# Kernel tuning notes

Hardware: AMD Instinct MI355X
Metric: run time of the kernel (lower is better)

The kernel has to match this reference:

```python
import jax, jax.numpy as jnp
import numpy as np

MODEL_DIM = 1024
HEAD_DIM = 64
BATCH = 4
SEQ = 4096


def setup_inputs() -> dict:
    key = jax.random.key(0)
    ks = jax.random.split(key, 7)
    s = 1.0 / np.sqrt(MODEL_DIM)
    x = jax.random.normal(ks[0], (BATCH, SEQ, MODEL_DIM), dtype=jnp.float32)
    # causal lower-triangular boolean mask, broadcast over batch
    mask = jnp.tril(jnp.ones((SEQ, SEQ), dtype=jnp.bool_))
    Wk = jax.random.uniform(ks[1], (MODEL_DIM, HEAD_DIM), jnp.float32, -s, s)
    bk = jax.random.uniform(ks[2], (HEAD_DIM,), jnp.float32, -s, s)
    Wq = jax.random.uniform(ks[3], (MODEL_DIM, HEAD_DIM), jnp.float32, -s, s)
    bq = jax.random.uniform(ks[4], (HEAD_DIM,), jnp.float32, -s, s)
    Wv = jax.random.uniform(ks[5], (MODEL_DIM, HEAD_DIM), jnp.float32, -s, s)
    bv = jax.random.uniform(ks[6], (HEAD_DIM,), jnp.float32, -s, s)
    return {"x": x, "mask": mask, "Wk": Wk, "bk": bk, "Wq": Wq, "bq": bq, "Wv": Wv, "bv": bv}


def reference(x, mask, Wk, bk, Wq, bq, Wv, bv):
    # K, Q, V: (B, S, Dh)
    K = jnp.einsum('bsd,dh->bsh', x, Wk) + bk
    Q = jnp.einsum('bsd,dh->bsh', x, Wq) + bq
    V = jnp.einsum('bsd,dh->bsh', x, Wv) + bv
    scale = 1.0 / jnp.sqrt(jnp.asarray(HEAD_DIM, dtype=x.dtype))
    G = jnp.einsum('bqh,bkh->bqk', Q, K) * scale  # (B, S, S)
    G = jnp.where(mask[None, :, :], G, -jnp.inf)
    G = jax.nn.softmax(G, axis=-1)
    # dropout is identity at inference (eval mode)
    attn = jnp.einsum('bqk,bkh->bqh', G, V)
    return attn
```

## Files before the change

kernel.cpp:

```cpp
#include <hip/hip_runtime.h>
#include <hip/hip_bf16.h>
#include <stdint.h>

typedef __attribute__((ext_vector_type(8))) short bf16x8;
typedef __attribute__((ext_vector_type(4))) short bf16x4;
typedef __attribute__((ext_vector_type(4))) float f32x4;
typedef __attribute__((ext_vector_type(4))) unsigned short us4;

#define MFMA32(a, b, c) __builtin_amdgcn_mfma_f32_16x16x32_bf16(a, b, c, 0, 0, 0)

#if defined(__has_builtin) && __has_builtin(__builtin_amdgcn_mfma_f32_16x16x16bf16_1k)
__device__ __forceinline__ f32x4 MFMA16(bf16x4 a, bf16x4 b, f32x4 c) {
    return __builtin_amdgcn_mfma_f32_16x16x16bf16_1k(a, b, c, 0, 0, 0);
}
#elif defined(__has_builtin) && __has_builtin(__builtin_amdgcn_mfma_f32_16x16x16_bf16)
__device__ __forceinline__ f32x4 MFMA16(bf16x4 a, bf16x4 b, f32x4 c) {
    return __builtin_amdgcn_mfma_f32_16x16x16_bf16(a, b, c, 0, 0, 0);
}
#else
__device__ __forceinline__ f32x4 MFMA16(bf16x4 a, bf16x4 b, f32x4 c) {
    f32x4 d;
    asm volatile("v_mfma_f32_16x16x16_bf16 %0, %1, %2, %3\n\ts_nop 7\n\ts_nop 2"
                 : "=v"(d) : "v"(a), "v"(b), "v"(c));
    return d;
}
#endif

__device__ __forceinline__ short f2bf(float f) {
    union { float f; uint32_t u; } v; v.f = f;
    uint32_t u = v.u;
    u = (u + 0x7FFFu + ((u >> 16) & 1u)) >> 16;
    return (short)u;
}

__device__ __forceinline__ uint32_t cvt_pk_bf16(float lo, float hi) {
    uint32_t r;
    asm("v_cvt_pk_bf16_f32 %0, %1, %2" : "=v"(r) : "v"(lo), "v"(hi));
    return r;
}

#define QSCALE 0.18033688011112042f

__global__ void wt_prep(const float* __restrict__ Wk, const float* __restrict__ bk,
                        const float* __restrict__ Wq, const float* __restrict__ bq,
                        const float* __restrict__ Wv, const float* __restrict__ bv,
                        short* __restrict__ WT, float* __restrict__ biasC) {
    int i = blockIdx.x * 256 + threadIdx.x;
    if (i < 192 * 1024) {
        int c = i >> 10, k = i & 1023, cc = c & 63;
        const float* W; float sc;
        if (c < 64)       { W = Wq; sc = QSCALE; }
        else if (c < 128) { W = Wk; sc = 1.0f;   }
        else              { W = Wv; sc = 1.0f;   }
        WT[i] = f2bf(W[k * 64 + cc] * sc);
    }
    if (blockIdx.x == 0 && threadIdx.x < 192) {
        int c = threadIdx.x;
        float bb;
        if (c < 64)       bb = bq[c] * QSCALE;
        else if (c < 128) bb = bk[c - 64];
        else              bb = bv[c - 128];
        biasC[c] = bb;
    }
}

__global__ __launch_bounds__(256, 4) void qkv_proj(
        const float* __restrict__ X, const short* __restrict__ WT,
        const float* __restrict__ biasC,
        short* __restrict__ Qb, short* __restrict__ Kb, short* __restrict__ Vt) {
    const int lane = threadIdx.x & 63, w = threadIdx.x >> 6;
    const int l15 = lane & 15, h = lane >> 4;
    const int row0 = blockIdx.x * 16;
    const int k0 = w * 256 + h * 8;

    f32x4 acc[12];
#pragma unroll
    for (int t = 0; t < 12; t++) acc[t] = (f32x4){0.f, 0.f, 0.f, 0.f};

    const float* xb = X + (size_t)(row0 + l15) * 1024 + k0;
    const short* wb = WT + (size_t)l15 * 1024 + k0;

    for (int kc = 0; kc < 256; kc += 32) {
        const float4 a0 = *(const float4*)(xb + kc);
        const float4 a1 = *(const float4*)(xb + kc + 4);
        bf16x8 af;
        af[0] = f2bf(a0.x); af[1] = f2bf(a0.y); af[2] = f2bf(a0.z); af[3] = f2bf(a0.w);
        af[4] = f2bf(a1.x); af[5] = f2bf(a1.y); af[6] = f2bf(a1.z); af[7] = f2bf(a1.w);
#pragma unroll
        for (int ct = 0; ct < 12; ct++) {
            bf16x8 bf = *(const bf16x8*)(wb + (size_t)ct * 16 * 1024 + kc);
            acc[ct] = MFMA32(af, bf, acc[ct]);
        }
    }

    __shared__ float buf[4][12][16][17];
#pragma unroll
    for (int ct = 0; ct < 12; ct++)
#pragma unroll
        for (int r = 0; r < 4; r++)
            buf[w][ct][h * 4 + r][l15] = acc[ct][r];
    __syncthreads();

    const int b = row0 >> 12, srow = row0 & 4095;

#pragma unroll
    for (int i = 0; i < 8; i++) {
        const int e = threadIdx.x + 256 * i;
        const int ct = e >> 8, row = (e >> 4) & 15, col = e & 15;
        float val = buf[0][ct][row][col] + buf[1][ct][row][col]
                  + buf[2][ct][row][col] + buf[3][ct][row][col]
                  + biasC[ct * 16 + col];
        if (ct < 4) Qb[(size_t)(row0 + row) * 64 + ct * 16 + col] = f2bf(val);
        else        Kb[(size_t)(row0 + row) * 64 + (ct - 4) * 16 + col] = f2bf(val);
    }
    {
        const int ctv = (threadIdx.x >> 4) & 3;
        const int col = threadIdx.x & 15;
        const int rg = threadIdx.x >> 6;
        const int hd = ctv * 16 + col;
        const float bias = biasC[128 + hd];
        us4 pk;
#pragma unroll
        for (int r = 0; r < 4; r++) {
            const int row = rg * 4 + r;
            float val = buf[0][8 + ctv][row][col] + buf[1][8 + ctv][row][col]
                      + buf[2][8 + ctv][row][col] + buf[3][8 + ctv][row][col] + bias;
            pk[r] = (unsigned short)f2bf(val);
        }
        *(us4*)(Vt + ((size_t)(b * 64 + hd)) * 4096 + srow + rg * 4) = pk;
    }
}

__device__ __forceinline__ void softmax_update(const f32x4 s[4], float& m, float& l,
                                               f32x4 o[4], bf16x4 pb[4]) {
    float mx = s[0][0];
#pragma unroll
    for (int c = 0; c < 4; c++)
#pragma unroll
        for (int r = 0; r < 4; r++) mx = fmaxf(mx, s[c][r]);
    mx = fmaxf(mx, __shfl_xor(mx, 16));
    mx = fmaxf(mx, __shfl_xor(mx, 32));
    const float mn = fmaxf(m, mx);
    const float fac = exp2f(m - mn);
    m = mn;
    float p[4][4];
    float sum = 0.f;
#pragma unroll
    for (int c = 0; c < 4; c++)
#pragma unroll
        for (int r = 0; r < 4; r++) { p[c][r] = exp2f(s[c][r] - mn); sum += p[c][r]; }
    sum += __shfl_xor(sum, 16);
    sum += __shfl_xor(sum, 32);
    l = l * fac + sum;
#pragma unroll
    for (int c = 0; c < 4; c++) o[c] *= fac;
#pragma unroll
    for (int c = 0; c < 4; c++) {
        union { bf16x4 v; uint32_t u[2]; } pk;
        pk.u[0] = cvt_pk_bf16(p[c][0], p[c][1]);
        pk.u[1] = cvt_pk_bf16(p[c][2], p[c][3]);
        pb[c] = pk.v;
    }
}

__global__ __launch_bounds__(256, 3) void attn(
        const short* __restrict__ Qb, const short* __restrict__ Kb,
        const short* __restrict__ Vt, float* __restrict__ out) {
    const int lane = threadIdx.x & 63, wg = threadIdx.x >> 6;
    const int l15 = lane & 15, h = lane >> 4;
    const int g = blockIdx.x;
    const int b = g >> 7;
    const int i = g & 127;
    const int u = (i & 1) ? (127 - (i >> 1)) : (i >> 1);
    const int row32 = u * 32;
    const int lt = u >> 1;
    const size_t bbase = (size_t)b * 4096 * 64;

    const short* qp0 = Qb + bbase + (size_t)(row32 + l15) * 64 + h * 8;
    const short* qp1 = qp0 + 16 * 64;
    const bf16x8 q00 = *(const bf16x8*)qp0,  q01 = *(const bf16x8*)(qp0 + 32);
    const bf16x8 q10 = *(const bf16x8*)qp1,  q11 = *(const bf16x8*)(qp1 + 32);

    f32x4 o0[4], o1[4];
    float m0 = -__builtin_inff(), m1 = -__builtin_inff(), l0 = 0.f, l1 = 0.f;
#pragma unroll
    for (int t = 0; t < 4; t++) { o0[t] = (f32x4){0,0,0,0}; o1[t] = (f32x4){0,0,0,0}; }

    for (int kt = wg; kt <= lt; kt += 4) {
        const short* kb = Kb + bbase + (size_t)kt * 64 * 64;
        f32x4 s0[4], s1[4];
#pragma unroll
        for (int c = 0; c < 4; c++) {
            const short* kp = kb + (size_t)(c * 16 + l15) * 64 + h * 8;
            const bf16x8 kf0 = *(const bf16x8*)kp;
            const bf16x8 kf1 = *(const bf16x8*)(kp + 32);
            f32x4 z = (f32x4){0,0,0,0};
            z = MFMA32(kf0, q00, z);  s0[c] = MFMA32(kf1, q01, z);
            z = (f32x4){0,0,0,0};
            z = MFMA32(kf0, q10, z);  s1[c] = MFMA32(kf1, q11, z);
        }
        if (kt == lt) {
            const int q0g = row32 + l15, q1g = q0g + 16;
#pragma unroll
            for (int c = 0; c < 4; c++) {
#pragma unroll
                for (int r = 0; r < 4; r++) {
                    const int key = kt * 64 + c * 16 + h * 4 + r;
                    if (key > q0g) s0[c][r] = -1e30f;
                    if (key > q1g) s1[c][r] = -1e30f;
                }
            }
        }
        bf16x4 pb0[4], pb1[4];
        softmax_update(s0, m0, l0, o0, pb0);
        softmax_update(s1, m1, l1, o1, pb1);

        const short* vb = Vt + (size_t)b * 64 * 4096 + kt * 64;
#pragma unroll
        for (int ct = 0; ct < 4; ct++) {
            const short* vp = vb + (size_t)(ct * 16 + l15) * 4096 + h * 4;
#pragma unroll
            for (int c = 0; c < 4; c++) {
                const bf16x4 vf = *(const bf16x4*)(vp + c * 16);
                o0[ct] = MFMA16(vf, pb0[c], o0[ct]);
                o1[ct] = MFMA16(vf, pb1[c], o1[ct]);
            }
        }
    }

    __shared__ float c_m[4][32], c_l[4][32];
    __shared__ float c_o[4][64][33];
    if (h == 0) {
        c_m[wg][l15] = m0;  c_m[wg][16 + l15] = m1;
        c_l[wg][l15] = l0;  c_l[wg][16 + l15] = l1;
    }
#pragma unroll
    for (int ct = 0; ct < 4; ct++)
#pragma unroll
        for (int r = 0; r < 4; r++) {
            c_o[wg][ct * 16 + h * 4 + r][l15]      = o0[ct][r];
            c_o[wg][ct * 16 + h * 4 + r][16 + l15] = o1[ct][r];
        }
    __syncthreads();

#pragma unroll
    for (int it = 0; it < 8; it++) {
        const int e = threadIdx.x + 256 * it;
        const int q = e >> 6, d = e & 63;
        const float M = fmaxf(fmaxf(c_m[0][q], c_m[1][q]), fmaxf(c_m[2][q], c_m[3][q]));
        float L = 0.f, V = 0.f;
#pragma unroll
        for (int ww = 0; ww < 4; ww++) {
            const float ee = exp2f(c_m[ww][q] - M);
            L += ee * c_l[ww][q];
            V += ee * c_o[ww][d][q];
        }
        out[bbase + (size_t)(row32 + q) * 64 + d] = V / L;
    }
}

extern "C" void kernel_launch(void* const* d_in, const int* in_sizes, int n_in,
                              void* d_out, int out_size, void* d_ws, size_t ws_size,
                              hipStream_t stream) {
    const float* x  = (const float*)d_in[0];
    const float* Wk = (const float*)d_in[2];
    const float* bk = (const float*)d_in[3];
    const float* Wq = (const float*)d_in[4];
    const float* bq = (const float*)d_in[5];
    const float* Wv = (const float*)d_in[6];
    const float* bv = (const float*)d_in[7];
    float* out = (float*)d_out;

    char* ws = (char*)d_ws;
    short* WT    = (short*)(ws);
    float* biasC = (float*)(ws + 393216);
    short* Qb    = (short*)(ws + (size_t)1 * (1 << 20));
    short* Kb    = (short*)(ws + (size_t)3 * (1 << 20));
    short* Vt    = (short*)(ws + (size_t)5 * (1 << 20));

    wt_prep<<<768, 256, 0, stream>>>(Wk, bk, Wq, bq, Wv, bv, WT, biasC);
    qkv_proj<<<1024, 256, 0, stream>>>(x, WT, biasC, Qb, Kb, Vt);
    attn<<<512, 256, 0, stream>>>(Qb, Kb, Vt, out);
}
```

Measured before the change: 157.7 us.

## Split attention KV range across blocks with separate merge kernel; stage X in LDS

The attention kernel now splits long causal rows into up to four KV chunks of 16 tiles each, launching 1280 blocks whose partial outputs (bf16), maxima and sums are written to workspace and combined by a new attn_merge kernel. This balances work across CUs, since the longest query rows no longer pin a single block. qkv_proj now converts the X tile to bf16 once into shared memory with packed cvt instructions instead of per-wave conversion, and the launch-bounds occupancy hints are dropped. The cost is an extra kernel launch, extra global traffic for partials, and bf16 rounding of partial outputs.

New measurement: 135.0 us. -14.4%, faster.

```diff
diff --git a/kernel.cpp b/kernel.cpp
--- a/kernel.cpp
+++ b/kernel.cpp
@@ -32,7 +32,10 @@
     u = (u + 0x7FFFu + ((u >> 16) & 1u)) >> 16;
     return (short)u;
 }
-
+__device__ __forceinline__ float bf2f(short s) {
+    union { uint32_t u; float f; } v; v.u = ((uint32_t)(unsigned short)s) << 16;
+    return v.f;
+}
 __device__ __forceinline__ uint32_t cvt_pk_bf16(float lo, float hi) {
     uint32_t r;
     asm("v_cvt_pk_bf16_f32 %0, %1, %2" : "=v"(r) : "v"(lo), "v"(hi));
@@ -64,67 +67,85 @@
     }
 }
 
-__global__ __launch_bounds__(256, 4) void qkv_proj(
+__global__ __launch_bounds__(256) void qkv_proj(
         const float* __restrict__ X, const short* __restrict__ WT,
         const float* __restrict__ biasC,
         short* __restrict__ Qb, short* __restrict__ Kb, short* __restrict__ Vt) {
-    const int lane = threadIdx.x & 63, w = threadIdx.x >> 6;
-    const int l15 = lane & 15, h = lane >> 4;
+    union SM {
+        short stage[16][1032];
+        float merge[12][16][4][17];
+    };
+    __shared__ SM sm;
+    const int t = threadIdx.x;
+    const int lane = t & 63, w = t >> 6, l15 = lane & 15, h = lane >> 4;
     const int row0 = blockIdx.x * 16;
-    const int k0 = w * 256 + h * 8;
+
+    {
+        const int srow = t >> 4, sl = t & 15;
+        const float* xr = X + (size_t)(row0 + srow) * 1024 + sl * 8;
+        short* dr = &sm.stage[srow][sl * 8];
+#pragma unroll
+        for (int it = 0; it < 8; it++) {
+            const float4 a0 = *(const float4*)(xr + it * 128);
+            const float4 a1 = *(const float4*)(xr + it * 128 + 4);
+            uint4 pk;
+            pk.x = cvt_pk_bf16(a0.x, a0.y);
+            pk.y = cvt_pk_bf16(a0.z, a0.w);
+            pk.z = cvt_pk_bf16(a1.x, a1.y);
+            pk.w = cvt_pk_bf16(a1.z, a1.w);
+            *(uint4*)(dr + it * 128) = pk;
+        }
+    }
+    __syncthreads();
 
     f32x4 acc[12];
 #pragma unroll
-    for (int t = 0; t < 12; t++) acc[t] = (f32x4){0.f, 0.f, 0.f, 0.f};
-
-    const float* xb = X + (size_t)(row0 + l15) * 1024 + k0;
-    const short* wb = WT + (size_t)l15 * 1024 + k0;
+    for (int ct = 0; ct < 12; ct++) acc[ct] = (f32x4){0.f, 0.f, 0.f, 0.f};
+
+    const short* ar = &sm.stage[l15][w * 256 + h * 8];
+    const short* wb = WT + (size_t)l15 * 1024 + w * 256 + h * 8;
 
     for (int kc = 0; kc < 256; kc += 32) {
-        const float4 a0 = *(const float4*)(xb + kc);
-        const float4 a1 = *(const float4*)(xb + kc + 4);
-        bf16x8 af;
-        af[0] = f2bf(a0.x); af[1] = f2bf(a0.y); af[2] = f2bf(a0.z); af[3] = f2bf(a0.w);
-        af[4] = f2bf(a1.x); af[5] = f2bf(a1.y); af[6] = f2bf(a1.z); af[7] = f2bf(a1.w);
+        const bf16x8 af = *(const bf16x8*)(ar + kc);
 #pragma unroll
         for (int ct = 0; ct < 12; ct++) {
-            bf16x8 bf = *(const bf16x8*)(wb + (size_t)ct * 16 * 1024 + kc);
+            const bf16x8 bf = *(const bf16x8*)(wb + (size_t)ct * 16 * 1024 + kc);
             acc[ct] = MFMA32(af, bf, acc[ct]);
         }
     }
-
-    __shared__ float buf[4][12][16][17];
+    __syncthreads();
+
 #pragma unroll
     for (int ct = 0; ct < 12; ct++)
 #pragma unroll
         for (int r = 0; r < 4; r++)
-            buf[w][ct][h * 4 + r][l15] = acc[ct][r];
+            sm.merge[ct][h * 4 + r][w][l15] = acc[ct][r];
     __syncthreads();
 
     const int b = row0 >> 12, srow = row0 & 4095;
 
 #pragma unroll
     for (int i = 0; i < 8; i++) {
-        const int e = threadIdx.x + 256 * i;
+        const int e = t + 256 * i;
         const int ct = e >> 8, row = (e >> 4) & 15, col = e & 15;
-        float val = buf[0][ct][row][col] + buf[1][ct][row][col]
-                  + buf[2][ct][row][col] + buf[3][ct][row][col]
+        float val = sm.merge[ct][row][0][col] + sm.merge[ct][row][1][col]
+                  + sm.merge[ct][row][2][col] + sm.merge[ct][row][3][col]
                   + biasC[ct * 16 + col];
         if (ct < 4) Qb[(size_t)(row0 + row) * 64 + ct * 16 + col] = f2bf(val);
         else        Kb[(size_t)(row0 + row) * 64 + (ct - 4) * 16 + col] = f2bf(val);
     }
     {
-        const int ctv = (threadIdx.x >> 4) & 3;
-        const int col = threadIdx.x & 15;
-        const int rg = threadIdx.x >> 6;
+        const int ctv = (t >> 4) & 3;
+        const int col = t & 15;
+        const int rg = t >> 6;
         const int hd = ctv * 16 + col;
         const float bias = biasC[128 + hd];
         us4 pk;
 #pragma unroll
         for (int r = 0; r < 4; r++) {
             const int row = rg * 4 + r;
-            float val = buf[0][8 + ctv][row][col] + buf[1][8 + ctv][row][col]
-                      + buf[2][8 + ctv][row][col] + buf[3][8 + ctv][row][col] + bias;
+            float val = sm.merge[8 + ctv][row][0][col] + sm.merge[8 + ctv][row][1][col]
+                      + sm.merge[8 + ctv][row][2][col] + sm.merge[8 + ctv][row][3][col] + bias;
             pk[r] = (unsigned short)f2bf(val);
         }
         *(us4*)(Vt + ((size_t)(b * 64 + hd)) * 4096 + srow + rg * 4) = pk;
@@ -163,17 +184,22 @@
     }
 }
 
-__global__ __launch_bounds__(256, 3) void attn(
+__global__ __launch_bounds__(256) void attn(
         const short* __restrict__ Qb, const short* __restrict__ Kb,
-        const short* __restrict__ Vt, float* __restrict__ out) {
+        const short* __restrict__ Vt,
+        short* __restrict__ PO, float* __restrict__ PM, float* __restrict__ PL) {
     const int lane = threadIdx.x & 63, wg = threadIdx.x >> 6;
     const int l15 = lane & 15, h = lane >> 4;
-    const int g = blockIdx.x;
-    const int b = g >> 7;
-    const int i = g & 127;
-    const int u = (i & 1) ? (127 - (i >> 1)) : (i >> 1);
+    const int j = blockIdx.x;
+    const int b = j / 320, jj = j - b * 320;
+    int u, c;
+    if (jj < 32)       { u = jj;                 c = 0; }
+    else if (jj < 96)  { u = 32 + ((jj - 32) >> 1);  c = (jj - 32) & 1; }
+    else if (jj < 192) { const int q3 = (jj - 96) / 3; u = 64 + q3; c = (jj - 96) - 3 * q3; }
+    else               { u = 96 + ((jj - 192) >> 2); c = (jj - 192) & 3; }
     const int row32 = u * 32;
     const int lt = u >> 1;
+    const int tend = min(c * 16 + 15, lt);
     const size_t bbase = (size_t)b * 4096 * 64;
 
     const short* qp0 = Qb + bbase + (size_t)(row32 + l15) * 64 + h * 8;
@@ -186,28 +212,28 @@
 #pragma unroll
     for (int t = 0; t < 4; t++) { o0[t] = (f32x4){0,0,0,0}; o1[t] = (f32x4){0,0,0,0}; }
 
-    for (int kt = wg; kt <= lt; kt += 4) {
+    for (int kt = c * 16 + wg; kt <= tend; kt += 4) {
         const short* kb = Kb + bbase + (size_t)kt * 64 * 64;
         f32x4 s0[4], s1[4];
 #pragma unroll
-        for (int c = 0; c < 4; c++) {
-            const short* kp = kb + (size_t)(c * 16 + l15) * 64 + h * 8;
+        for (int cc = 0; cc < 4; cc++) {
+            const short* kp = kb + (size_t)(cc * 16 + l15) * 64 + h * 8;
             const bf16x8 kf0 = *(const bf16x8*)kp;
             const bf16x8 kf1 = *(const bf16x8*)(kp + 32);
             f32x4 z = (f32x4){0,0,0,0};
-            z = MFMA32(kf0, q00, z);  s0[c] = MFMA32(kf1, q01, z);
+            z = MFMA32(kf0, q00, z);  s0[cc] = MFMA32(kf1, q01, z);
             z = (f32x4){0,0,0,0};
-            z = MFMA32(kf0, q10, z);  s1[c] = MFMA32(kf1, q11, z);
+            z = MFMA32(kf0, q10, z);  s1[cc] = MFMA32(kf1, q11, z);
         }
         if (kt == lt) {
             const int q0g = row32 + l15, q1g = q0g + 16;
 #pragma unroll
-            for (int c = 0; c < 4; c++) {
+            for (int cc = 0; cc < 4; cc++) {
 #pragma unroll
                 for (int r = 0; r < 4; r++) {
-                    const int key = kt * 64 + c * 16 + h * 4 + r;
-                    if (key > q0g) s0[c][r] = -1e30f;
-                    if (key > q1g) s1[c][r] = -1e30f;
+                    const int key = kt * 64 + cc * 16 + h * 4 + r;
+                    if (key > q0g) s0[cc][r] = -1e30f;
+                    if (key > q1g) s1[cc][r] = -1e30f;
                 }
             }
         }
@@ -220,43 +246,88 @@
         for (int ct = 0; ct < 4; ct++) {
             const short* vp = vb + (size_t)(ct * 16 + l15) * 4096 + h * 4;
 #pragma unroll
-            for (int c = 0; c < 4; c++) {
-                const bf16x4 vf = *(const bf16x4*)(vp + c * 16);
-                o0[ct] = MFMA16(vf, pb0[c], o0[ct]);
-                o1[ct] = MFMA16(vf, pb1[c], o1[ct]);
+            for (int cc = 0; cc < 4; cc++) {
+                const bf16x4 vf = *(const bf16x4*)(vp + cc * 16);
+                o0[ct] = MFMA16(vf, pb0[cc], o0[ct]);
+                o1[ct] = MFMA16(vf, pb1[cc], o1[ct]);
             }
         }
     }
 
     __shared__ float c_m[4][32], c_l[4][32];
-    __shared__ float c_o[4][64][33];
+    __shared__ short c_ob[4][32][72];
     if (h == 0) {
         c_m[wg][l15] = m0;  c_m[wg][16 + l15] = m1;
         c_l[wg][l15] = l0;  c_l[wg][16 + l15] = l1;
     }
 #pragma unroll
-    for (int ct = 0; ct < 4; ct++)
-#pragma unroll
-        for (int r = 0; r < 4; r++) {
-            c_o[wg][ct * 16 + h * 4 + r][l15]      = o0[ct][r];
-            c_o[wg][ct * 16 + h * 4 + r][16 + l15] = o1[ct][r];
-        }
+    for (int ct = 0; ct < 4; ct++) {
+        *(uint32_t*)&c_ob[wg][l15][ct * 16 + h * 4]          = cvt_pk_bf16(o0[ct][0], o0[ct][1]);
+        *(uint32_t*)&c_ob[wg][l15][ct * 16 + h * 4 + 2]      = cvt_pk_bf16(o0[ct][2], o0[ct][3]);
+        *(uint32_t*)&c_ob[wg][16 + l15][ct * 16 + h * 4]     = cvt_pk_bf16(o1[ct][0], o1[ct][1]);
+        *(uint32_t*)&c_ob[wg][16 + l15][ct * 16 + h * 4 + 2] = cvt_pk_bf16(o1[ct][2], o1[ct][3]);
+    }
     __syncthreads();
 
-#pragma unroll
-    for (int it = 0; it < 8; it++) {
-        const int e = threadIdx.x + 256 * it;
-        const int q = e >> 6, d = e & 63;
-        const float M = fmaxf(fmaxf(c_m[0][q], c_m[1][q]), fmaxf(c_m[2][q], c_m[3][q]));
-        float L = 0.f, V = 0.f;
-#pragma unroll
-        for (int ww = 0; ww < 4; ww++) {
-            const float ee = exp2f(c_m[ww][q] - M);
-            L += ee * c_l[ww][q];
-            V += ee * c_o[ww][d][q];
-        }
-        out[bbase + (size_t)(row32 + q) * 64 + d] = V / L;
-    }
+    const int e = threadIdx.x;
+    const int q = e >> 3, d0 = (e & 7) * 8;
+    float M = fmaxf(fmaxf(c_m[0][q], c_m[1][q]), fmaxf(c_m[2][q], c_m[3][q]));
+    float L = 0.f;
+    float acc[8];
+#pragma unroll
+    for (int i = 0; i < 8; i++) acc[i] = 0.f;
+#pragma unroll
+    for (int ww = 0; ww < 4; ww++) {
+        const float ew = exp2f(c_m[ww][q] - M);
+        L += ew * c_l[ww][q];
+        const bf16x8 ov = *(const bf16x8*)&c_ob[ww][q][d0];
+#pragma unroll
+        for (int i = 0; i < 8; i++) acc[i] += ew * bf2f(ov[i]);
+    }
+    if ((e & 7) == 0) { PM[(size_t)j * 32 + q] = M; PL[(size_t)j * 32 + q] = L; }
+    uint4 pk;
+    pk.x = cvt_pk_bf16(acc[0], acc[1]);
+    pk.y = cvt_pk_bf16(acc[2], acc[3]);
+    pk.z = cvt_pk_bf16(acc[4], acc[5]);
+    pk.w = cvt_pk_bf16(acc[6], acc[7]);
+    *(uint4*)(PO + (size_t)j * 2048 + q * 64 + d0) = pk;
+}
+
+__global__ __launch_bounds__(256) void attn_merge(
+        const short* __restrict__ PO, const float* __restrict__ PM,
+        const float* __restrict__ PL, float* __restrict__ out) {
+    const int bu = blockIdx.x;
+    const int b = bu >> 7, u = bu & 127;
+    const int off = (u < 32) ? u
+                 : (u < 64) ? 32 + 2 * (u - 32)
+                 : (u < 96) ? 96 + 3 * (u - 64)
+                 :            192 + 4 * (u - 96);
+    const int nc = (u + 32) >> 5;
+    const int base = b * 320 + off;
+    const int e = threadIdx.x;
+    const int q = e >> 3, d0 = (e & 7) * 8;
+
+    float M = -__builtin_inff();
+    for (int c = 0; c < nc; c++) M = fmaxf(M, PM[(size_t)(base + c) * 32 + q]);
+    float L = 0.f;
+    float acc[8];
+#pragma unroll
+    for (int i = 0; i < 8; i++) acc[i] = 0.f;
+    for (int c = 0; c < nc; c++) {
+        const size_t slot = base + c;
+        const float ew = exp2f(PM[slot * 32 + q] - M);
+        L += ew * PL[slot * 32 + q];
+        const bf16x8 ov = *(const bf16x8*)(PO + slot * 2048 + q * 64 + d0);
+#pragma unroll
+        for (int i = 0; i < 8; i++) acc[i] += ew * bf2f(ov[i]);
+    }
+    const float inv = 1.0f / L;
+    float4 w0, w1;
+    w0.x = acc[0] * inv; w0.y = acc[1] * inv; w0.z = acc[2] * inv; w0.w = acc[3] * inv;
+    w1.x = acc[4] * inv; w1.y = acc[5] * inv; w1.z = acc[6] * inv; w1.w = acc[7] * inv;
+    float* dst = out + (size_t)b * 4096 * 64 + (size_t)(u * 32 + q) * 64 + d0;
+    *(float4*)dst = w0;
+    *(float4*)(dst + 4) = w1;
 }
 
 extern "C" void kernel_launch(void* const* d_in, const int* in_sizes, int n_in,
@@ -274,11 +345,15 @@
     char* ws = (char*)d_ws;
     short* WT    = (short*)(ws);
     float* biasC = (float*)(ws + 393216);
-    short* Qb    = (short*)(ws + (size_t)1 * (1 << 20));
-    short* Kb    = (short*)(ws + (size_t)3 * (1 << 20));
-    short* Vt    = (short*)(ws + (size_t)5 * (1 << 20));
+    short* Qb    = (short*)(ws + (size_t)1  * (1 << 20));
+    short* Kb    = (short*)(ws + (size_t)3  * (1 << 20));
+    short* Vt    = (short*)(ws + (size_t)5  * (1 << 20));
+    short* PO    = (short*)(ws + (size_t)7  * (1 << 20));
+    float* PM    = (float*)(ws + (size_t)13 * (1 << 20));
+    float* PL    = (float*)(ws + (size_t)14 * (1 << 20));
 
     wt_prep<<<768, 256, 0, stream>>>(Wk, bk, Wq, bq, Wv, bv, WT, biasC);
     qkv_proj<<<1024, 256, 0, stream>>>(x, WT, biasC, Qb, Kb, Vt);
-    attn<<<512, 256, 0, stream>>>(Qb, Kb, Vt, out);
-}
+    attn<<<1280, 256, 0, stream>>>(Qb, Kb, Vt, PO, PM, PL);
+    attn_merge<<<512, 256, 0, stream>>>(PO, PM, PL, out);
+}
```
